# Optimization experiments

Measured on AMD Instinct MI355X. Metric: run time of the kernel, lower is better.

## Reference

```python
import jax, jax.numpy as jnp
import numpy as np

B, N, D, H, K = 8, 128, 256, 128, 8

def setup_inputs() -> dict:
    key = jax.random.key(0)
    ks = jax.random.split(key, 6)
    E = jax.random.normal(ks[0], (B, N, D), dtype=jnp.float32)
    # kaiming_uniform-like init for linear weights
    lim1 = np.sqrt(6.0 / (2 * D))
    W1 = jax.random.uniform(ks[1], (H, 2 * D), minval=-lim1, maxval=lim1, dtype=jnp.float32)
    b1 = jnp.zeros((H,), dtype=jnp.float32)
    lim2 = np.sqrt(6.0 / H)
    W2 = jax.random.uniform(ks[2], (D, H), minval=-lim2, maxval=lim2, dtype=jnp.float32)
    b2 = jnp.zeros((D,), dtype=jnp.float32)
    q = jax.random.normal(ks[3], (K, D), dtype=jnp.float32) * (1.0 / D ** 0.5)
    return {"E": E, "W1": W1, "b1": b1, "W2": W2, "b2": b2, "q": q}

def reference(E, W1, b1, W2, b2, q):
    # phi(cat(Ei,Ej)) == relu(E_i @ W1a^T + E_j @ W1b^T + b1) @ W2^T + b2
    # Split first linear's weight to avoid materializing the [B,N,N,2D] concat.
    W1a, W1b = W1[:, :D], W1[:, D:]          # each [H, D]
    Ai = jnp.einsum('bnd,hd->bnh', E, W1a)   # [B,N,H] (row half)
    Aj = jnp.einsum('bnd,hd->bnh', E, W1b)   # [B,N,H] (col half)
    hidden = jax.nn.relu(Ai[:, :, None, :] + Aj[:, None, :, :] + b1)  # [B,N,N,H]
    # dropout is identity at inference
    # Fuse second linear with query dot: (hidden @ W2^T + b2) . q_h
    #   = hidden @ (W2^T q_h) + b2.q_h
    Wq = jnp.einsum('dh,kd->hk', W2, q)      # [H, K]
    bq = jnp.einsum('d,kd->k', b2, q)        # [K]
    logits = jnp.einsum('bijh,hk->bijh'[:0] or 'bijh,hk->bijk', hidden, Wq) + bq  # [B,N,N,K]
    M = jax.nn.sigmoid(logits).transpose(0, 3, 1, 2)  # [B,K,N,N]
    eye = jnp.eye(N, dtype=M.dtype)[None, None]
    return M * (1.0 - eye)
```

## Files before the change

kernel.cpp:

```cpp
#include <hip/hip_runtime.h>
#include <hip/hip_bf16.h>

#define PB 8
#define PN 128
#define PD 256
#define PH 128
#define PK 8

__global__ __launch_bounds__(256) void k1_proj(
        const float* __restrict__ E, const float* __restrict__ W1,
        const float* __restrict__ b1, const float* __restrict__ W2,
        const float* __restrict__ b2, const float* __restrict__ q,
        float* __restrict__ Ai, float* __restrict__ Aj,
        float* __restrict__ Wq, float* __restrict__ bq)
{
    const int blk = blockIdx.x;
    const int t = threadIdx.x;

    if (blk < PB * PN) {
        __shared__ float es[PD];
        es[t] = E[blk * PD + t];
        __syncthreads();

        const int h = t & (PH - 1);
        const int part = t >> 7;
        const float* wrow = W1 + h * (2 * PD) + part * PD;

        float acc = 0.f;
        #pragma unroll 4
        for (int d0 = 0; d0 < PD; d0 += 8) {
            float w[8], e[8];
            *reinterpret_cast<float4*>(&w[0]) = *reinterpret_cast<const float4*>(wrow + d0);
            *reinterpret_cast<float4*>(&w[4]) = *reinterpret_cast<const float4*>(wrow + d0 + 4);
            *reinterpret_cast<float4*>(&e[0]) = *reinterpret_cast<const float4*>(&es[d0]);
            *reinterpret_cast<float4*>(&e[4]) = *reinterpret_cast<const float4*>(&es[d0 + 4]);
            #pragma unroll
            for (int r = 0; r < 8; ++r) acc = fmaf(w[r], e[r], acc);
        }
        if (part == 0) Ai[blk * PH + h] = acc + b1[h];
        else           Aj[blk * PH + h] = acc;
    } else {
        const int k = blk - PB * PN;
        __shared__ float qs[PD];
        __shared__ float red[256];
        qs[t] = q[k * PD + t];
        __syncthreads();

        if (t < PH) {
            float acc = 0.f;
            for (int d = 0; d < PD; ++d)
                acc = fmaf(W2[d * PH + t], qs[d], acc);
            Wq[t * PK + k] = acc;
        }
        red[t] = b2[t] * qs[t];
        __syncthreads();
        for (int s = 128; s > 0; s >>= 1) {
            if (t < s) red[t] += red[t + s];
            __syncthreads();
        }
        if (t == 0) bq[k] = red[0];
    }
}

__global__ __launch_bounds__(128) void k2_score(
        const float* __restrict__ Ai, const float* __restrict__ Aj,
        const float* __restrict__ Wq, const float* __restrict__ bq,
        float* __restrict__ out)
{
    const int b = blockIdx.x >> 7;
    const int i = blockIdx.x & (PN - 1);
    const int j = threadIdx.x;

    const float* airow = Ai + (b * PN + i) * PH;
    const float* ajrow = Aj + (b * PN + j) * PH;

    float acc[PK];
    #pragma unroll
    for (int k = 0; k < PK; ++k) acc[k] = bq[k];

    #pragma unroll 2
    for (int h = 0; h < PH; h += 4) {
        float ai4[4], aj4[4];
        *reinterpret_cast<float4*>(ai4) = *reinterpret_cast<const float4*>(airow + h);
        *reinterpret_cast<float4*>(aj4) = *reinterpret_cast<const float4*>(ajrow + h);
        #pragma unroll
        for (int r = 0; r < 4; ++r) {
            float v = fmaxf(ai4[r] + aj4[r], 0.f);
            float w[8];
            *reinterpret_cast<float4*>(&w[0]) = *reinterpret_cast<const float4*>(Wq + (h + r) * PK);
            *reinterpret_cast<float4*>(&w[4]) = *reinterpret_cast<const float4*>(Wq + (h + r) * PK + 4);
            #pragma unroll
            for (int k = 0; k < PK; ++k) acc[k] = fmaf(v, w[k], acc[k]);
        }
    }

    #pragma unroll
    for (int k = 0; k < PK; ++k) {
        float s = 1.f / (1.f + __expf(-acc[k]));
        if (j == i) s = 0.f;
        out[((b * PK + k) * PN + i) * PN + j] = s;
    }
}

extern "C" void kernel_launch(void* const* d_in, const int* in_sizes, int n_in,
                              void* d_out, int out_size, void* d_ws, size_t ws_size,
                              hipStream_t stream) {
    const float* E  = (const float*)d_in[0];
    const float* W1 = (const float*)d_in[1];
    const float* b1 = (const float*)d_in[2];
    const float* W2 = (const float*)d_in[3];
    const float* b2 = (const float*)d_in[4];
    const float* q  = (const float*)d_in[5];

    float* Ai = (float*)d_ws;
    float* Aj = Ai + PB * PN * PH;
    float* Wq = Aj + PB * PN * PH;
    float* bq = Wq + PH * PK;

    k1_proj<<<PB * PN + PK, 256, 0, stream>>>(E, W1, b1, W2, b2, q, Ai, Aj, Wq, bq);
    k2_score<<<PB * PN, 128, 0, stream>>>(Ai, Aj, Wq, bq, (float*)d_out);
}
```

Baseline: 109.2 us.

## Transpose W1 and Aj layouts, tile projection over rows, widen score blocks

Adds a prep kernel that transposes W1, so the projection kernel can read weights coalesced and reuse each weight load across four E rows held in registers. Aj is stored transposed, so score threads read it coalesced along j, and score blocks now cover two rows i with 256 threads. The sigmoid uses a hardware reciprocal. The cost is a third kernel launch and an extra weight transpose on every call, and E is now read through uniform scalar-like loads.

```diff
diff --git a/kernel.cpp b/kernel.cpp
--- a/kernel.cpp
+++ b/kernel.cpp
@@ -1,102 +1,106 @@
 #include <hip/hip_runtime.h>
-#include <hip/hip_bf16.h>
 
 #define PB 8
 #define PN 128
 #define PD 256
 #define PH 128
 #define PK 8
+#define D2 (2*PD)
+#define NT 4
 
-__global__ __launch_bounds__(256) void k1_proj(
-        const float* __restrict__ E, const float* __restrict__ W1,
-        const float* __restrict__ b1, const float* __restrict__ W2,
+__global__ __launch_bounds__(128) void t0_prep(
+        const float* __restrict__ W1, const float* __restrict__ W2,
         const float* __restrict__ b2, const float* __restrict__ q,
-        float* __restrict__ Ai, float* __restrict__ Aj,
-        float* __restrict__ Wq, float* __restrict__ bq)
+        float* __restrict__ W1t, float* __restrict__ Wq, float* __restrict__ bq)
 {
-    const int blk = blockIdx.x;
-    const int t = threadIdx.x;
-
-    if (blk < PB * PN) {
-        __shared__ float es[PD];
-        es[t] = E[blk * PD + t];
+    const int blk = blockIdx.x, t = threadIdx.x;
+    if (blk < D2) {
+        W1t[blk * PH + t] = W1[t * D2 + blk];
+    } else {
+        const int k = blk - D2;
+        __shared__ float qs[PD];
+        __shared__ float red[128];
+        qs[t]       = q[k * PD + t];
+        qs[t + 128] = q[k * PD + t + 128];
         __syncthreads();
-
-        const int h = t & (PH - 1);
-        const int part = t >> 7;
-        const float* wrow = W1 + h * (2 * PD) + part * PD;
-
         float acc = 0.f;
         #pragma unroll 4
-        for (int d0 = 0; d0 < PD; d0 += 8) {
-            float w[8], e[8];
-            *reinterpret_cast<float4*>(&w[0]) = *reinterpret_cast<const float4*>(wrow + d0);
-            *reinterpret_cast<float4*>(&w[4]) = *reinterpret_cast<const float4*>(wrow + d0 + 4);
-            *reinterpret_cast<float4*>(&e[0]) = *reinterpret_cast<const float4*>(&es[d0]);
-            *reinterpret_cast<float4*>(&e[4]) = *reinterpret_cast<const float4*>(&es[d0 + 4]);
-            #pragma unroll
-            for (int r = 0; r < 8; ++r) acc = fmaf(w[r], e[r], acc);
-        }
-        if (part == 0) Ai[blk * PH + h] = acc + b1[h];
-        else           Aj[blk * PH + h] = acc;
-    } else {
-        const int k = blk - PB * PN;
-        __shared__ float qs[PD];
-        __shared__ float red[256];
-        qs[t] = q[k * PD + t];
+        for (int d = 0; d < PD; ++d)
+            acc = fmaf(W2[d * PH + t], qs[d], acc);
+        Wq[t * PK + k] = acc;
+        red[t] = b2[t] * qs[t] + b2[t + 128] * qs[t + 128];
         __syncthreads();
-
-        if (t < PH) {
-            float acc = 0.f;
-            for (int d = 0; d < PD; ++d)
-                acc = fmaf(W2[d * PH + t], qs[d], acc);
-            Wq[t * PK + k] = acc;
-        }
-        red[t] = b2[t] * qs[t];
-        __syncthreads();
-        for (int s = 128; s > 0; s >>= 1) {
-            if (t < s) red[t] += red[t + s];
-            __syncthreads();
-        }
+        for (int s = 64; s > 0; s >>= 1) { if (t < s) red[t] += red[t + s]; __syncthreads(); }
         if (t == 0) bq[k] = red[0];
     }
 }
 
-__global__ __launch_bounds__(128) void k2_score(
-        const float* __restrict__ Ai, const float* __restrict__ Aj,
+__global__ __launch_bounds__(256) void k1_proj(
+        const float* __restrict__ E, const float* __restrict__ W1t,
+        const float* __restrict__ b1,
+        float* __restrict__ Ai, float* __restrict__ Ajt)
+{
+    const int blk = blockIdx.x, t = threadIdx.x;
+    const int b  = blk / (PN / NT);
+    const int n0 = (blk % (PN / NT)) * NT;
+    const int h = t & (PH - 1);
+    const int part = t >> 7;
+
+    const float* w = W1t + part * PD * PH + h;
+    const float* e = E + (b * PN + n0) * PD;
+
+    float acc[NT];
+    #pragma unroll
+    for (int n = 0; n < NT; ++n) acc[n] = 0.f;
+
+    #pragma unroll 8
+    for (int d = 0; d < PD; ++d) {
+        const float wv = w[d * PH];
+        #pragma unroll
+        for (int n = 0; n < NT; ++n)
+            acc[n] = fmaf(wv, e[n * PD + d], acc[n]);
+    }
+
+    if (part == 0) {
+        const float bb = b1[h];
+        #pragma unroll
+        for (int n = 0; n < NT; ++n)
+            Ai[(b * PN + n0 + n) * PH + h] = acc[n] + bb;
+    } else {
+        #pragma unroll
+        for (int n = 0; n < NT; ++n)
+            Ajt[(b * PH + h) * PN + n0 + n] = acc[n];
+    }
+}
+
+__global__ __launch_bounds__(256) void k2_score(
+        const float* __restrict__ Ai, const float* __restrict__ Ajt,
         const float* __restrict__ Wq, const float* __restrict__ bq,
         float* __restrict__ out)
 {
-    const int b = blockIdx.x >> 7;
-    const int i = blockIdx.x & (PN - 1);
-    const int j = threadIdx.x;
+    const int blk = blockIdx.x, t = threadIdx.x;
+    const int b = blk >> 6;
+    const int i = ((blk & 63) << 1) + (t >> 7);
+    const int j = t & (PN - 1);
 
-    const float* airow = Ai + (b * PN + i) * PH;
-    const float* ajrow = Aj + (b * PN + j) * PH;
+    const float* ai = Ai + (b * PN + i) * PH;
+    const float* aj = Ajt + b * PH * PN + j;
 
     float acc[PK];
     #pragma unroll
     for (int k = 0; k < PK; ++k) acc[k] = bq[k];
 
-    #pragma unroll 2
-    for (int h = 0; h < PH; h += 4) {
-        float ai4[4], aj4[4];
-        *reinterpret_cast<float4*>(ai4) = *reinterpret_cast<const float4*>(airow + h);
-        *reinterpret_cast<float4*>(aj4) = *reinterpret_cast<const float4*>(ajrow + h);
+    #pragma unroll 4
+    for (int h = 0; h < PH; ++h) {
+        const float v = fmaxf(ai[h] + aj[h * PN], 0.f);
         #pragma unroll
-        for (int r = 0; r < 4; ++r) {
-            float v = fmaxf(ai4[r] + aj4[r], 0.f);
-            float w[8];
-            *reinterpret_cast<float4*>(&w[0]) = *reinterpret_cast<const float4*>(Wq + (h + r) * PK);
-            *reinterpret_cast<float4*>(&w[4]) = *reinterpret_cast<const float4*>(Wq + (h + r) * PK + 4);
-            #pragma unroll
-            for (int k = 0; k < PK; ++k) acc[k] = fmaf(v, w[k], acc[k]);
-        }
+        for (int k = 0; k < PK; ++k)
+            acc[k] = fmaf(v, Wq[h * PK + k], acc[k]);
     }
 
     #pragma unroll
     for (int k = 0; k < PK; ++k) {
-        float s = 1.f / (1.f + __expf(-acc[k]));
+        float s = __builtin_amdgcn_rcpf(1.f + __expf(-acc[k]));
         if (j == i) s = 0.f;
         out[((b * PK + k) * PN + i) * PN + j] = s;
     }
@@ -112,11 +116,13 @@
     const float* b2 = (const float*)d_in[4];
     const float* q  = (const float*)d_in[5];
 
-    float* Ai = (float*)d_ws;
-    float* Aj = Ai + PB * PN * PH;
-    float* Wq = Aj + PB * PN * PH;
-    float* bq = Wq + PH * PK;
+    float* Ai  = (float*)d_ws;
+    float* Ajt = Ai + PB * PN * PH;
+    float* W1t = Ajt + PB * PN * PH;
+    float* Wq  = W1t + D2 * PH;
+    float* bq  = Wq + PH * PK;
 
-    k1_proj<<<PB * PN + PK, 256, 0, stream>>>(E, W1, b1, W2, b2, q, Ai, Aj, Wq, bq);
-    k2_score<<<PB * PN, 128, 0, stream>>>(Ai, Aj, Wq, bq, (float*)d_out);
+    t0_prep<<<D2 + PK, 128, 0, stream>>>(W1, W2, b2, q, W1t, Wq, bq);
+    k1_proj<<<PB * (PN / NT), 256, 0, stream>>>(E, W1t, b1, Ai, Ajt);
+    k2_score<<<PB * PN / 2, 256, 0, stream>>>(Ai, Ajt, Wq, bq, (float*)d_out);
 }
```

Result: no change. 107.5 us (-1.6%).
